# Kernel optimization log

Measured on AMD Instinct MI355X. Metric: run time of the kernel, lower is better.

## Reference

```python
import jax, jax.numpy as jnp
import numpy as np

B, N, K, PC, NC = 4, 4096, 20, 6, 13


def setup_inputs() -> dict:
    key = jax.random.key(0)
    ks = jax.random.split(key, 32)
    dims = [(12, 64), (64, 64), (128, 64), (64, 64), (128, 64), (192, 1024), (1216, 512), (512, 256)]
    inp = {"x": jax.random.normal(ks[0], (B, N, PC), jnp.float32)}
    for j, (ci, co) in enumerate(dims, 1):
        inp[f"w{j}"] = jax.random.normal(ks[j], (co, ci), jnp.float32) * (1.0 / np.sqrt(ci))
        # BatchNorm (eval mode) folded to per-channel affine: y = h*s + b
        inp[f"s{j}"] = jnp.ones((co,), jnp.float32) + 0.01 * jax.random.normal(ks[10 + j], (co,), jnp.float32)
        inp[f"b{j}"] = 0.01 * jax.random.normal(ks[20 + j], (co,), jnp.float32)
    inp["w9"] = jax.random.normal(ks[30], (NC, 256), jnp.float32) * (1.0 / np.sqrt(256))
    inp["b9"] = 0.01 * jax.random.normal(ks[31], (NC,), jnp.float32)
    return inp


def _lrelu(h):
    return jnp.where(h >= 0, h, 0.2 * h)


def _knn_idx(y, k):
    # y: (B, C, N); pairwise_distance = -||xi - xj||^2, topk -> nearest neighbors
    xx = jnp.sum(y * y, axis=1)                       # (B, N)
    inner = jnp.einsum('bcn,bcm->bnm', y, y)          # (B, N, N)
    pd = 2.0 * inner - xx[:, :, None] - xx[:, None, :]
    return jax.lax.top_k(pd, k)[1]                    # (B, N, k) int32


def _graph_feature(y, k):
    # y: (B, C, N) -> edge features (B, 2C, N, k): concat(neighbor - x, x)
    idx = _knn_idx(y, k)
    yt = jnp.transpose(y, (0, 2, 1))                  # (B, N, C)
    nb = jax.vmap(lambda f, i: f[i])(yt, idx)         # (B, N, k, C)
    c = yt[:, :, None, :]
    feat = jnp.concatenate([nb - c, jnp.broadcast_to(c, nb.shape)], axis=-1)
    return jnp.transpose(feat, (0, 3, 1, 2))          # (B, 2C, N, k)


def _conv2(f, w, s, b):
    # 1x1 Conv2d (no bias) + folded BN + LeakyReLU(0.2)
    h = jnp.einsum('oc,bcnk->bonk', w, f)
    return _lrelu(h * s[None, :, None, None] + b[None, :, None, None])


def _conv1(f, w, s, b):
    h = jnp.einsum('oc,bcn->bon', w, f)
    return _lrelu(h * s[None, :, None] + b[None, :, None])


def _forward(x, w1, s1, b1, w2, s2, b2, w3, s3, b3, w4, s4, b4, w5, s5, b5,
             w6, s6, b6, w7, s7, b7, w8, s8, b8, w9, b9):
    y = jnp.transpose(x, (0, 2, 1))                   # (B, C, N)
    f = _graph_feature(y, K)
    h = _conv2(f, w1, s1, b1)
    h = _conv2(h, w2, s2, b2)
    x1 = h.max(axis=-1)                               # (B, 64, N)
    f = _graph_feature(x1, K)
    h = _conv2(f, w3, s3, b3)
    h = _conv2(h, w4, s4, b4)
    x2 = h.max(axis=-1)
    f = _graph_feature(x2, K)
    h = _conv2(f, w5, s5, b5)
    x3 = h.max(axis=-1)
    cat = jnp.concatenate([x1, x2, x3], axis=1)       # (B, 192, N)
    g = _conv1(cat, w6, s6, b6).max(axis=-1, keepdims=True)  # (B, 1024, 1)
    g = jnp.broadcast_to(g, (g.shape[0], g.shape[1], x1.shape[-1]))
    h = jnp.concatenate([g, x1, x2, x3], axis=1)      # (B, 1216, N)
    h = _conv1(h, w7, s7, b7)
    h = _conv1(h, w8, s8, b8)
    # dropout is identity in eval mode
    out = jnp.einsum('oc,bcn->bon', w9, h) + b9[None, :, None]
    return out                                        # (B, NC, N)


def reference(x, w1, s1, b1, w2, s2, b2, w3, s3, b3, w4, s4, b4, w5, s5, b5,
              w6, s6, b6, w7, s7, b7, w8, s8, b8, w9, b9):
    return _forward(x, w1, s1, b1, w2, s2, b2, w3, s3, b3, w4, s4, b4, w5, s5, b5,
                    w6, s6, b6, w7, s7, b7, w8, s8, b8, w9, b9)
```

## Files before the change

kernel.cpp:

```cpp
#include <hip/hip_runtime.h>
#include <hip/hip_bf16.h>
#include <cstdint>
#include <cstddef>

#define NB 4
#define NPTS 4096
#define KK 20

typedef unsigned int u32;
typedef unsigned long long u64;

__device__ __forceinline__ float lrelu(float v) { return v >= 0.f ? v : 0.2f * v; }

__device__ __forceinline__ u32 fmap(float f) {
  u32 u = __float_as_uint(f);
  return (int)u < 0 ? ~u : (u | 0x80000000u);
}

__device__ __forceinline__ u64 wmax64(u64 v) {
#pragma unroll
  for (int o = 32; o >= 1; o >>= 1) {
    u64 t = __shfl_xor(v, o, 64);
    v = t > v ? t : v;
  }
  return v;
}

template <int C>
__global__ void k_sq(const float* __restrict__ f, float* __restrict__ xx) {
  int p = blockIdx.x * 256 + threadIdx.x;
  const float* fp = f + (size_t)p * C;
  float s = 0.f;
  if constexpr ((C & 3) == 0) {
#pragma unroll
    for (int c = 0; c < C; c += 4) {
      float4 v = *reinterpret_cast<const float4*>(fp + c);
      s += v.x * v.x + v.y * v.y + v.z * v.z + v.w * v.w;
    }
  } else {
#pragma unroll
    for (int c = 0; c < C; c++) s += fp[c] * fp[c];
  }
  xx[p] = s;
}

__global__ __launch_bounds__(512) void k_knn6(const float* __restrict__ f,
                                              const float* __restrict__ xx,
                                              int* __restrict__ idxo,
                                              int* __restrict__ flg) {
  __shared__ float chunkl[6 * 65];
  const int tid = threadIdx.x, wv = tid >> 6, lane = tid & 63;
  const int row = blockIdx.x * 8 + wv;
  const int b = row >> 12;
  const float xi = xx[row];

  float y[6];
#pragma unroll
  for (int c = 0; c < 6; c++) y[c] = f[(size_t)row * 6 + c];

  u64 t0 = 0, t1 = 0, t2 = 0, t3 = 0;

  for (int jc = 0; jc < NPTS / 64; jc++) {
    __syncthreads();
    for (int t = tid; t < 64 * 6; t += 512) {
      int j = t / 6, c = t - j * 6;
      chunkl[c * 65 + j] = f[(size_t)(b * NPTS + jc * 64 + j) * 6 + c];
    }
    __syncthreads();
    const float xj = xx[b * NPTS + jc * 64 + lane];
    float acc = 0.f;
#pragma unroll
    for (int c = 0; c < 6; c++) acc = fmaf(chunkl[c * 65 + lane], y[c], acc);
    const float s = fmaf(2.f, acc, -xi) - xj;
    const u64 key = ((u64)fmap(s) << 32) | (u64)(~(u32)(jc * 64 + lane));
    if (key > t3) {
      u64 a0 = t0, a1 = t1, a2 = t2;
      bool g0 = key > a0, g1 = key > a1, g2 = key > a2;
      t0 = g0 ? key : a0;
      t1 = g0 ? a0 : (g1 ? key : a1);
      t2 = g1 ? a1 : (g2 ? key : a2);
      t3 = g2 ? a2 : key;
    }
  }

  u64 h = t0, n1 = t1, n2 = t2, n3 = t3;
  int pops = 0, myj = 0;
  for (int m = 0; m < KK; m++) {
    u64 wm = wmax64(h);
    int j = (int)(~(u32)wm) & (NPTS - 1);
    if (lane == m) myj = j;
    if (h == wm) { h = n1; n1 = n2; n2 = n3; n3 = 0; pops++; }
  }
  u64 bad = __ballot(pops >= 4);
  if (lane < KK) idxo[(size_t)row * KK + lane] = myj;
  if (lane == 0) flg[row] = (bad != 0ull) ? 1 : 0;
}

__global__ __launch_bounds__(256, 2) void k_knn64(const float* __restrict__ f,
                                                  const float* __restrict__ xx,
                                                  int* __restrict__ idxo,
                                                  int* __restrict__ flg) {
  __shared__ float ch[2][64 * 68];
  __shared__ float ypl[16 * 68];
  const int tid = threadIdx.x, wv = tid >> 6, lane = tid & 63;
  const int rowbase = blockIdx.x * 16;
  const int b = rowbase >> 12;
  const float* fb = f + (size_t)b * NPTS * 64;
  const int r0 = rowbase + wv * 4;

  {
    int row = tid >> 4, q = tid & 15;
    float4 v = *reinterpret_cast<const float4*>(f + (size_t)(rowbase + row) * 64 + 4 * q);
    *reinterpret_cast<float4*>(&ypl[row * 68 + 4 * q]) = v;
  }
  float xi[4];
#pragma unroll
  for (int r = 0; r < 4; r++) xi[r] = xx[r0 + r];

  u64 t0[4], t1[4], t2[4], t3[4];
#pragma unroll
  for (int r = 0; r < 4; r++) { t0[r] = 0; t1[r] = 0; t2[r] = 0; t3[r] = 0; }

#pragma unroll 1
  for (int jp = 0; jp < NPTS / 128; jp++) {
#pragma unroll 1
    for (int k = 0; k < 8; k++) {
      int flat = k * 256 + tid;
      int row = flat >> 4, q = flat & 15;
      float4 v = *reinterpret_cast<const float4*>(
          fb + (size_t)(jp * 128 + row) * 64 + 4 * q);
      *reinterpret_cast<float4*>(&ch[row >> 6][(row & 63) * 68 + 4 * q]) = v;
    }
    __syncthreads();

    float acc[4][2];
#pragma unroll
    for (int r = 0; r < 4; r++) { acc[r][0] = 0.f; acc[r][1] = 0.f; }
#pragma unroll 2
    for (int q = 0; q < 16; q++) {
      const float4 c0 = *reinterpret_cast<const float4*>(&ch[0][lane * 68 + 4 * q]);
      const float4 c1 = *reinterpret_cast<const float4*>(&ch[1][lane * 68 + 4 * q]);
#pragma unroll
      for (int r = 0; r < 4; r++) {
        const float4 yq = *reinterpret_cast<const float4*>(&ypl[(wv * 4 + r) * 68 + 4 * q]);
        acc[r][0] = fmaf(c0.x, yq.x, acc[r][0]);
        acc[r][0] = fmaf(c0.y, yq.y, acc[r][0]);
        acc[r][0] = fmaf(c0.z, yq.z, acc[r][0]);
        acc[r][0] = fmaf(c0.w, yq.w, acc[r][0]);
        acc[r][1] = fmaf(c1.x, yq.x, acc[r][1]);
        acc[r][1] = fmaf(c1.y, yq.y, acc[r][1]);
        acc[r][1] = fmaf(c1.z, yq.z, acc[r][1]);
        acc[r][1] = fmaf(c1.w, yq.w, acc[r][1]);
      }
    }
    const float xj0 = xx[b * NPTS + jp * 128 + lane];
    const float xj1 = xx[b * NPTS + jp * 128 + 64 + lane];
    const u32 j0 = ~(u32)(jp * 128 + lane);
    const u32 j1 = ~(u32)(jp * 128 + 64 + lane);
#pragma unroll
    for (int r = 0; r < 4; r++) {
      {
        const float s = fmaf(2.f, acc[r][0], -xi[r]) - xj0;
        const u64 key = ((u64)fmap(s) << 32) | (u64)j0;
        if (key > t3[r]) {
          u64 a0 = t0[r], a1 = t1[r], a2 = t2[r];
          bool g0 = key > a0, g1 = key > a1, g2 = key > a2;
          t0[r] = g0 ? key : a0;
          t1[r] = g0 ? a0 : (g1 ? key : a1);
          t2[r] = g1 ? a1 : (g2 ? key : a2);
          t3[r] = g2 ? a2 : key;
        }
      }
      {
        const float s = fmaf(2.f, acc[r][1], -xi[r]) - xj1;
        const u64 key = ((u64)fmap(s) << 32) | (u64)j1;
        if (key > t3[r]) {
          u64 a0 = t0[r], a1 = t1[r], a2 = t2[r];
          bool g0 = key > a0, g1 = key > a1, g2 = key > a2;
          t0[r] = g0 ? key : a0;
          t1[r] = g0 ? a0 : (g1 ? key : a1);
          t2[r] = g1 ? a1 : (g2 ? key : a2);
          t3[r] = g2 ? a2 : key;
        }
      }
    }
    __syncthreads();
  }

#pragma unroll
  for (int r = 0; r < 4; r++) {
    u64 h = t0[r], n1 = t1[r], n2 = t2[r], n3 = t3[r];
    int pops = 0, myj = 0;
    for (int m = 0; m < KK; m++) {
      u64 wm = wmax64(h);
      int j = (int)(~(u32)wm) & (NPTS - 1);
      if (lane == m) myj = j;
      if (h == wm) { h = n1; n1 = n2; n2 = n3; n3 = 0; pops++; }
    }
    u64 bad = __ballot(pops >= 4);
    if (lane < KK) idxo[(size_t)(r0 + r) * KK + lane] = myj;
    if (lane == 0) flg[r0 + r] = (bad != 0ull) ? 1 : 0;
  }
}

template <int C>
__global__ __launch_bounds__(64) void k_knn_fix(const float* __restrict__ f,
                                                const float* __restrict__ xx,
                                                int* __restrict__ idxo,
                                                const int* __restrict__ flg) {
  __shared__ u64 kl[NPTS];
  const int lane = threadIdx.x;
  for (int row = blockIdx.x; row < NB * NPTS; row += gridDim.x) {
    if (!flg[row]) continue;
    const int b = row >> 12;
    float yreg[C];
#pragma unroll
    for (int c = 0; c < C; c++) yreg[c] = f[(size_t)row * C + c];
    const float xi = xx[row];
    for (int jj = 0; jj < 64; jj++) {
      int j = jj * 64 + lane;
      const float* fp = f + (size_t)(b * NPTS + j) * C;
      float d = 0.f;
#pragma unroll
      for (int c = 0; c < C; c++) d = fmaf(yreg[c], fp[c], d);
      float s = fmaf(2.f, d, -xi) - xx[b * NPTS + j];
      kl[j] = ((u64)fmap(s) << 32) | (u64)(u32)(~(u32)j);
    }
    __syncthreads();
    int myj = 0;
    for (int m = 0; m < KK; m++) {
      u64 lm = 0;
      for (int jj = 0; jj < 64; jj++) {
        u64 v = kl[jj * 64 + lane];
        lm = v > lm ? v : lm;
      }
      u64 wm = wmax64(lm);
      int j = (int)(~(u32)wm) & (NPTS - 1);
      if (lane == m) myj = j;
      if (lane == (j & 63)) kl[j] = 0;
      __syncthreads();
    }
    if (lane < KK) idxo[row * KK + lane] = myj;
    __syncthreads();
  }
}

__global__ __launch_bounds__(256) void k_ec1(
    const float* __restrict__ x, const int* __restrict__ idx,
    const float* __restrict__ w1, const float* __restrict__ s1, const float* __restrict__ b1,
    const float* __restrict__ w2, const float* __restrict__ s2, const float* __restrict__ b2,
    float* __restrict__ out) {
  __shared__ float h1l[4][64];
  const int wv = threadIdx.x >> 6, lane = threadIdx.x & 63;
  float w1r[12];
#pragma unroll
  for (int c = 0; c < 12; c += 4) {
    float4 v = *reinterpret_cast<const float4*>(w1 + lane * 12 + c);
    w1r[c] = v.x; w1r[c + 1] = v.y; w1r[c + 2] = v.z; w1r[c + 3] = v.w;
  }
  float w2r[64];
#pragma unroll
  for (int c = 0; c < 64; c += 4) {
    float4 v = *reinterpret_cast<const float4*>(w2 + lane * 64 + c);
    w2r[c] = v.x; w2r[c + 1] = v.y; w2r[c + 2] = v.z; w2r[c + 3] = v.w;
  }
  const float sc1 = s1[lane], bc1 = b1[lane], sc2 = s2[lane], bc2 = b2[lane];
  const int wid = blockIdx.x * 4 + wv;
  for (int p = wid; p < NB * NPTS; p += 2048) {
    const float* cp = x + (size_t)p * 6;
    float c0 = cp[0], c1 = cp[1], c2 = cp[2], c3 = cp[3], c4 = cp[4], c5 = cp[5];
    const int bb = p >> 12;
    float m = -3.402823466e38f;
    for (int k = 0; k < KK; k++) {
      int nb = idx[p * KK + k];
      const float* nf = x + (size_t)((bb << 12) + nb) * 6;
      float e0 = nf[0] - c0, e1 = nf[1] - c1, e2 = nf[2] - c2;
      float e3 = nf[3] - c3, e4 = nf[4] - c4, e5 = nf[5] - c5;
      float h = w1r[0] * e0 + w1r[1] * e1 + w1r[2] * e2 + w1r[3] * e3 + w1r[4] * e4 +
                w1r[5] * e5 + w1r[6] * c0 + w1r[7] * c1 + w1r[8] * c2 + w1r[9] * c3 +
                w1r[10] * c4 + w1r[11] * c5;
      h = lrelu(fmaf(h, sc1, bc1));
      h1l[wv][lane] = h;
      __syncthreads();
      float a0 = 0.f, a1 = 0.f;
#pragma unroll
      for (int c = 0; c < 64; c += 8) {
        float4 hv = *reinterpret_cast<const float4*>(&h1l[wv][c]);
        float4 hw = *reinterpret_cast<const float4*>(&h1l[wv][c + 4]);
        a0 = fmaf(w2r[c], hv.x, a0); a0 = fmaf(w2r[c + 1], hv.y, a0);
        a0 = fmaf(w2r[c + 2], hv.z, a0); a0 = fmaf(w2r[c + 3], hv.w, a0);
        a1 = fmaf(w2r[c + 4], hw.x, a1); a1 = fmaf(w2r[c + 5], hw.y, a1);
        a1 = fmaf(w2r[c + 6], hw.z, a1); a1 = fmaf(w2r[c + 7], hw.w, a1);
      }
      m = fmaxf(m, lrelu(fmaf(a0 + a1, sc2, bc2)));
      __syncthreads();
    }
    out[(size_t)p * 64 + lane] = m;
  }
}

template <bool HAS2>
__global__ __launch_bounds__(256, 1) void k_ec2(
    const float* __restrict__ xin, const int* __restrict__ idx,
    const float* __restrict__ w3, const float* __restrict__ s3, const float* __restrict__ b3,
    const float* __restrict__ w4, const float* __restrict__ s4, const float* __restrict__ b4,
    float* __restrict__ out) {
  __shared__ float ctl[4][64];
  __shared__ float nbl[4][64];
  __shared__ float h1l[4][64];
  const int wv = threadIdx.x >> 6, lane = threadIdx.x & 63;
  float wa[64], wb[64];
#pragma unroll
  for (int c = 0; c < 64; c += 4) {
    float4 va = *reinterpret_cast<const float4*>(w3 + (size_t)lane * 128 + c);
    float4 vb = *reinterpret_cast<const float4*>(w3 + (size_t)lane * 128 + 64 + c);
    wa[c] = va.x; wa[c + 1] = va.y; wa[c + 2] = va.z; wa[c + 3] = va.w;
    wb[c] = vb.x - va.x; wb[c + 1] = vb.y - va.y; wb[c + 2] = vb.z - va.z; wb[c + 3] = vb.w - va.w;
  }
  float w4r[64];
  if constexpr (HAS2) {
#pragma unroll
    for (int c = 0; c < 64; c += 4) {
      float4 v = *reinterpret_cast<const float4*>(w4 + (size_t)lane * 64 + c);
      w4r[c] = v.x; w4r[c + 1] = v.y; w4r[c + 2] = v.z; w4r[c + 3] = v.w;
    }
  }
  const float sc3 = s3[lane], bc3 = b3[lane];
  float sc4 = 0.f, bc4 = 0.f;
  if constexpr (HAS2) { sc4 = s4[lane]; bc4 = b4[lane]; }
  const int wid = blockIdx.x * 4 + wv;
  for (int p = wid; p < NB * NPTS; p += 2048) {
    const int bb = p >> 12;
    ctl[wv][lane] = xin[(size_t)p * 64 + lane];
    __syncthreads();
    float d0 = 0.f, d1 = 0.f;
#pragma unroll
    for (int c = 0; c < 64; c += 8) {
      float4 cv = *reinterpret_cast<const float4*>(&ctl[wv][c]);
      float4 cw = *reinterpret_cast<const float4*>(&ctl[wv][c + 4]);
      d0 = fmaf(wb[c], cv.x, d0); d0 = fmaf(wb[c + 1], cv.y, d0);
      d0 = fmaf(wb[c + 2], cv.z, d0); d0 = fmaf(wb[c + 3], cv.w, d0);
      d1 = fmaf(wb[c + 4], cw.x, d1); d1 = fmaf(wb[c + 5], cw.y, d1);
      d1 = fmaf(wb[c + 6], cw.z, d1); d1 = fmaf(wb[c + 7], cw.w, d1);
    }
    const float cd = d0 + d1;
    float m = -3.402823466e38f;
    for (int k = 0; k < KK; k++) {
      int nb = idx[p * KK + k];
      nbl[wv][lane] = xin[(size_t)((bb << 12) + nb) * 64 + lane];
      __syncthreads();
      float a0 = cd, a1 = 0.f;
#pragma unroll
      for (int c = 0; c < 64; c += 8) {
        float4 nv = *reinterpret_cast<const float4*>(&nbl[wv][c]);
        float4 nw = *reinterpret_cast<const float4*>(&nbl[wv][c + 4]);
        a0 = fmaf(wa[c], nv.x, a0); a0 = fmaf(wa[c + 1], nv.y, a0);
        a0 = fmaf(wa[c + 2], nv.z, a0); a0 = fmaf(wa[c + 3], nv.w, a0);
        a1 = fmaf(wa[c + 4], nw.x, a1); a1 = fmaf(wa[c + 5], nw.y, a1);
        a1 = fmaf(wa[c + 6], nw.z, a1); a1 = fmaf(wa[c + 7], nw.w, a1);
      }
      float h = lrelu(fmaf(a0 + a1, sc3, bc3));
      if constexpr (HAS2) {
        h1l[wv][lane] = h;
        __syncthreads();
        float q0 = 0.f, q1 = 0.f;
#pragma unroll
        for (int c = 0; c < 64; c += 8) {
          float4 hv = *reinterpret_cast<const float4*>(&h1l[wv][c]);
          float4 hw = *reinterpret_cast<const float4*>(&h1l[wv][c + 4]);
          q0 = fmaf(w4r[c], hv.x, q0); q0 = fmaf(w4r[c + 1], hv.y, q0);
          q0 = fmaf(w4r[c + 2], hv.z, q0); q0 = fmaf(w4r[c + 3], hv.w, q0);
          q1 = fmaf(w4r[c + 4], hw.x, q1); q1 = fmaf(w4r[c + 5], hw.y, q1);
          q1 = fmaf(w4r[c + 6], hw.z, q1); q1 = fmaf(w4r[c + 7], hw.w, q1);
        }
        m = fmaxf(m, lrelu(fmaf(q0 + q1, sc4, bc4)));
        __syncthreads();
      } else {
        m = fmaxf(m, h);
        __syncthreads();
      }
    }
    out[(size_t)p * 64 + lane] = m;
    __syncthreads();
  }
}

__global__ __launch_bounds__(256, 1) void k_conv6(
    const float* __restrict__ x1, const float* __restrict__ x2, const float* __restrict__ x3,
    const float* __restrict__ w6, const float* __restrict__ s6, const float* __restrict__ b6,
    float* __restrict__ gpart) {
  __shared__ float fl[192];
  const int tid = threadIdx.x;
  const int cg = blockIdx.x & 3;
  const int ch = (blockIdx.x >> 2) & 31;
  const int b = blockIdx.x >> 7;
  const int co = cg * 256 + tid;
  float wr[192];
#pragma unroll
  for (int c = 0; c < 192; c += 4) {
    float4 v = *reinterpret_cast<const float4*>(w6 + (size_t)co * 192 + c);
    wr[c] = v.x; wr[c + 1] = v.y; wr[c + 2] = v.z; wr[c + 3] = v.w;
  }
  const float sc = s6[co], bc = b6[co];
  float m = -3.402823466e38f;
  for (int pp = 0; pp < 128; pp++) {
    const int p = b * NPTS + ch * 128 + pp;
    if (tid < 192) {
      fl[tid] = tid < 64 ? x1[(size_t)p * 64 + tid]
              : tid < 128 ? x2[(size_t)p * 64 + tid - 64]
                          : x3[(size_t)p * 64 + tid - 128];
    }
    __syncthreads();
    float a0 = 0.f, a1 = 0.f, a2 = 0.f, a3 = 0.f;
#pragma unroll
    for (int c = 0; c < 192; c += 16) {
      float4 f0 = *reinterpret_cast<const float4*>(&fl[c]);
      float4 f1 = *reinterpret_cast<const float4*>(&fl[c + 4]);
      float4 f2 = *reinterpret_cast<const float4*>(&fl[c + 8]);
      float4 f3 = *reinterpret_cast<const float4*>(&fl[c + 12]);
      a0 = fmaf(wr[c], f0.x, a0); a0 = fmaf(wr[c + 1], f0.y, a0);
      a0 = fmaf(wr[c + 2], f0.z, a0); a0 = fmaf(wr[c + 3], f0.w, a0);
      a1 = fmaf(wr[c + 4], f1.x, a1); a1 = fmaf(wr[c + 5], f1.y, a1);
      a1 = fmaf(wr[c + 6], f1.z, a1); a1 = fmaf(wr[c + 7], f1.w, a1);
      a2 = fmaf(wr[c + 8], f2.x, a2); a2 = fmaf(wr[c + 9], f2.y, a2);
      a2 = fmaf(wr[c + 10], f2.z, a2); a2 = fmaf(wr[c + 11], f2.w, a2);
      a3 = fmaf(wr[c + 12], f3.x, a3); a3 = fmaf(wr[c + 13], f3.y, a3);
      a3 = fmaf(wr[c + 14], f3.z, a3); a3 = fmaf(wr[c + 15], f3.w, a3);
    }
    m = fmaxf(m, lrelu(fmaf((a0 + a1) + (a2 + a3), sc, bc)));
    __syncthreads();
  }
  gpart[(size_t)(b * 32 + ch) * 1024 + co] = m;
}

__global__ void k_gred(const float* __restrict__ gpart, float* __restrict__ g) {
  int t = blockIdx.x * 256 + threadIdx.x;
  int b = t >> 10, co = t & 1023;
  float m = -3.402823466e38f;
  for (int ch = 0; ch < 32; ch++) m = fmaxf(m, gpart[(size_t)(b * 32 + ch) * 1024 + co]);
  g[t] = m;
}

__global__ void k_gc(const float* __restrict__ w7, const float* __restrict__ g,
                     float* __restrict__ gcv) {
  int t = blockIdx.x * 256 + threadIdx.x;
  int b = t >> 9, co = t & 511;
  const float* gr = g + b * 1024;
  const float* wr = w7 + (size_t)co * 1216;
  float a0 = 0.f, a1 = 0.f, a2 = 0.f, a3 = 0.f;
  for (int ci = 0; ci < 1024; ci += 4) {
    float4 wv = *reinterpret_cast<const float4*>(wr + ci);
    float4 gv = *reinterpret_cast<const float4*>(gr + ci);
    a0 = fmaf(wv.x, gv.x, a0); a1 = fmaf(wv.y, gv.y, a1);
    a2 = fmaf(wv.z, gv.z, a2); a3 = fmaf(wv.w, gv.w, a3);
  }
  gcv[t] = (a0 + a1) + (a2 + a3);
}

__global__ __launch_bounds__(256, 1) void k_conv7(
    const float* __restrict__ x1, const float* __restrict__ x2, const float* __restrict__ x3,
    const float* __restrict__ gcv, const float* __restrict__ w7,
    const float* __restrict__ s7, const float* __restrict__ b7,
    float* __restrict__ h7, int bbase) {
  __shared__ float fl[192];
  const int tid = threadIdx.x;
  const int wv = tid >> 6, lane = tid & 63;
  const int cohalf = blockIdx.x & 1;
  const int ch = (blockIdx.x >> 1) & 63;
  const int bloc = blockIdx.x >> 7;
  const int b = bbase + bloc;
  const int co = (cohalf * 4 + wv) * 64 + lane;
  float wr[192];
#pragma unroll
  for (int c = 0; c < 192; c += 4) {
    float4 v = *reinterpret_cast<const float4*>(w7 + (size_t)co * 1216 + 1024 + c);
    wr[c] = v.x; wr[c + 1] = v.y; wr[c + 2] = v.z; wr[c + 3] = v.w;
  }
  const float sc = s7[co], bc = b7[co], g0 = gcv[b * 512 + co];
  for (int pp = 0; pp < 64; pp++) {
    const int p = b * NPTS + ch * 64 + pp;
    if (tid < 192) {
      fl[tid] = tid < 64 ? x1[(size_t)p * 64 + tid]
              : tid < 128 ? x2[(size_t)p * 64 + tid - 64]
                          : x3[(size_t)p * 64 + tid - 128];
    }
    __syncthreads();
    float a0 = g0, a1 = 0.f, a2 = 0.f, a3 = 0.f;
#pragma unroll
    for (int c = 0; c < 192; c += 16) {
      float4 f0 = *reinterpret_cast<const float4*>(&fl[c]);
      float4 f1 = *reinterpret_cast<const float4*>(&fl[c + 4]);
      float4 f2 = *reinterpret_cast<const float4*>(&fl[c + 8]);
      float4 f3 = *reinterpret_cast<const float4*>(&fl[c + 12]);
      a0 = fmaf(wr[c], f0.x, a0); a0 = fmaf(wr[c + 1], f0.y, a0);
      a0 = fmaf(wr[c + 2], f0.z, a0); a0 = fmaf(wr[c + 3], f0.w, a0);
      a1 = fmaf(wr[c + 4], f1.x, a1); a1 = fmaf(wr[c + 5], f1.y, a1);
      a1 = fmaf(wr[c + 6], f1.z, a1); a1 = fmaf(wr[c + 7], f1.w, a1);
      a2 = fmaf(wr[c + 8], f2.x, a2); a2 = fmaf(wr[c + 9], f2.y, a2);
      a2 = fmaf(wr[c + 10], f2.z, a2); a2 = fmaf(wr[c + 11], f2.w, a2);
      a3 = fmaf(wr[c + 12], f3.x, a3); a3 = fmaf(wr[c + 13], f3.y, a3);
      a3 = fmaf(wr[c + 14], f3.z, a3); a3 = fmaf(wr[c + 15], f3.w, a3);
    }
    h7[(size_t)(bloc * NPTS + ch * 64 + pp) * 512 + co] =
        lrelu(fmaf((a0 + a1) + (a2 + a3), sc, bc));
    __syncthreads();
  }
}

__global__ __launch_bounds__(256) void k_conv8(
    const float* __restrict__ h7, const float* __restrict__ w8,
    const float* __restrict__ s8, const float* __restrict__ b8,
    float* __restrict__ h8, int bbase) {
  __shared__ float Wl[64 * 68];
  __shared__ float Xl[64 * 68];
  const int tid = threadIdx.x;
  const int cot = blockIdx.x & 3;
  const int nt = blockIdx.x >> 2;
  const int co0 = (tid & 15) * 4;
  const int n0 = (tid >> 4) * 4;
  const int sr = tid >> 2;
  const int sci = (tid & 3) * 16;
  float acc[4][4];
#pragma unroll
  for (int i = 0; i < 4; i++)
#pragma unroll
    for (int j = 0; j < 4; j++) acc[i][j] = 0.f;

  for (int cib = 0; cib < 512; cib += 64) {
    __syncthreads();
    {
      const float* ws_ = w8 + (size_t)(cot * 64 + sr) * 512 + cib + sci;
#pragma unroll
      for (int s = 0; s < 16; s += 4) {
        float4 v = *reinterpret_cast<const float4*>(ws_ + s);
        Wl[(sci + s) * 68 + sr] = v.x;
        Wl[(sci + s + 1) * 68 + sr] = v.y;
        Wl[(sci + s + 2) * 68 + sr] = v.z;
        Wl[(sci + s + 3) * 68 + sr] = v.w;
      }
      const float* xs = h7 + (size_t)(nt * 64 + sr) * 512 + cib + sci;
#pragma unroll
      for (int s = 0; s < 16; s += 4) {
        float4 v = *reinterpret_cast<const float4*>(xs + s);
        Xl[(sci + s) * 68 + sr] = v.x;
        Xl[(sci + s + 1) * 68 + sr] = v.y;
        Xl[(sci + s + 2) * 68 + sr] = v.z;
        Xl[(sci + s + 3) * 68 + sr] = v.w;
      }
    }
    __syncthreads();
#pragma unroll 8
    for (int ci = 0; ci < 64; ci++) {
      float4 wv = *reinterpret_cast<const float4*>(&Wl[ci * 68 + co0]);
      float4 xv = *reinterpret_cast<const float4*>(&Xl[ci * 68 + n0]);
      acc[0][0] = fmaf(wv.x, xv.x, acc[0][0]);
      acc[0][1] = fmaf(wv.x, xv.y, acc[0][1]);
      acc[0][2] = fmaf(wv.x, xv.z, acc[0][2]);
      acc[0][3] = fmaf(wv.x, xv.w, acc[0][3]);
      acc[1][0] = fmaf(wv.y, xv.x, acc[1][0]);
      acc[1][1] = fmaf(wv.y, xv.y, acc[1][1]);
      acc[1][2] = fmaf(wv.y, xv.z, acc[1][2]);
      acc[1][3] = fmaf(wv.y, xv.w, acc[1][3]);
      acc[2][0] = fmaf(wv.z, xv.x, acc[2][0]);
      acc[2][1] = fmaf(wv.z, xv.y, acc[2][1]);
      acc[2][2] = fmaf(wv.z, xv.z, acc[2][2]);
      acc[2][3] = fmaf(wv.z, xv.w, acc[2][3]);
      acc[3][0] = fmaf(wv.w, xv.x, acc[3][0]);
      acc[3][1] = fmaf(wv.w, xv.y, acc[3][1]);
      acc[3][2] = fmaf(wv.w, xv.z, acc[3][2]);
      acc[3][3] = fmaf(wv.w, xv.w, acc[3][3]);
    }
  }
  float scv[4], bcv[4];
#pragma unroll
  for (int i = 0; i < 4; i++) {
    scv[i] = s8[cot * 64 + co0 + i];
    bcv[i] = b8[cot * 64 + co0 + i];
  }
#pragma unroll
  for (int j = 0; j < 4; j++) {
    float4 o;
    o.x = lrelu(fmaf(acc[0][j], scv[0], bcv[0]));
    o.y = lrelu(fmaf(acc[1][j], scv[1], bcv[1]));
    o.z = lrelu(fmaf(acc[2][j], scv[2], bcv[2]));
    o.w = lrelu(fmaf(acc[3][j], scv[3], bcv[3]));
    *reinterpret_cast<float4*>(
        &h8[(size_t)(bbase * NPTS + nt * 64 + n0 + j) * 256 + cot * 64 + co0]) = o;
  }
}

__global__ __launch_bounds__(256) void k_conv9(const float* __restrict__ h8,
                                               const float* __restrict__ w9,
                                               const float* __restrict__ b9,
                                               float* __restrict__ outp) {
  __shared__ float Wl[16 * 256];
  __shared__ float Xl[64 * 68];
  const int tid = threadIdx.x;
  for (int q = tid; q < 16 * 256; q += 256) Wl[q] = q < 13 * 256 ? w9[q] : 0.f;
  const int p = tid & 63, cg = tid >> 6;
  const int sr = tid >> 2, sci = (tid & 3) * 16;
  float acc[4] = {0.f, 0.f, 0.f, 0.f};
  for (int cib = 0; cib < 256; cib += 64) {
    __syncthreads();
    {
      const float* xs = h8 + (size_t)(blockIdx.x * 64 + sr) * 256 + cib + sci;
#pragma unroll
      for (int s = 0; s < 16; s += 4) {
        float4 v = *reinterpret_cast<const float4*>(xs + s);
        Xl[(sci + s) * 68 + sr] = v.x;
        Xl[(sci + s + 1) * 68 + sr] = v.y;
        Xl[(sci + s + 2) * 68 + sr] = v.z;
        Xl[(sci + s + 3) * 68 + sr] = v.w;
      }
    }
    __syncthreads();
#pragma unroll 8
    for (int ci = 0; ci < 64; ci++) {
      float xv = Xl[ci * 68 + p];
#pragma unroll
      for (int q = 0; q < 4; q++)
        acc[q] = fmaf(Wl[(cg * 4 + q) * 256 + cib + ci], xv, acc[q]);
    }
  }
  const int pg = blockIdx.x * 64 + p;
  const int bb = pg >> 12, n = pg & (NPTS - 1);
#pragma unroll
  for (int q = 0; q < 4; q++) {
    int co = cg * 4 + q;
    if (co < 13) outp[(size_t)(bb * 13 + co) * NPTS + n] = acc[q] + b9[co];
  }
}

extern "C" void kernel_launch(void* const* d_in, const int* in_sizes, int n_in,
                              void* d_out, int out_size, void* d_ws, size_t ws_size,
                              hipStream_t stream) {
  const float* x = (const float*)d_in[0];
  const float* w1 = (const float*)d_in[1];
  const float* s1 = (const float*)d_in[2];
  const float* b1 = (const float*)d_in[3];
  const float* w2 = (const float*)d_in[4];
  const float* s2 = (const float*)d_in[5];
  const float* b2 = (const float*)d_in[6];
  const float* w3 = (const float*)d_in[7];
  const float* s3 = (const float*)d_in[8];
  const float* b3 = (const float*)d_in[9];
  const float* w4 = (const float*)d_in[10];
  const float* s4 = (const float*)d_in[11];
  const float* b4 = (const float*)d_in[12];
  const float* w5 = (const float*)d_in[13];
  const float* s5 = (const float*)d_in[14];
  const float* b5 = (const float*)d_in[15];
  const float* w6 = (const float*)d_in[16];
  const float* s6 = (const float*)d_in[17];
  const float* b6 = (const float*)d_in[18];
  const float* w7 = (const float*)d_in[19];
  const float* s7 = (const float*)d_in[20];
  const float* b7 = (const float*)d_in[21];
  const float* w8 = (const float*)d_in[22];
  const float* s8 = (const float*)d_in[23];
  const float* b8 = (const float*)d_in[24];
  const float* w9 = (const float*)d_in[25];
  const float* b9 = (const float*)d_in[26];

  float* ws = (float*)d_ws;
  float* xxp = ws + 0;
  int* idxp = (int*)(ws + 16384);
  int* flg = (int*)(ws + 344064);
  float* x1 = ws + 360448;
  float* x2 = ws + 1409024;
  float* x3 = ws + 2457600;
  float* gpart = ws + 3506176;
  float* g = ws + 3637248;
  float* gcv = ws + 3641344;
  float* h7 = ws + 3643392;
  float* h8 = ws + 7837696;

  k_sq<6><<<64, 256, 0, stream>>>(x, xxp);
  k_knn6<<<2048, 512, 0, stream>>>(x, xxp, idxp, flg);
  k_knn_fix<6><<<512, 64, 0, stream>>>(x, xxp, idxp, flg);
  k_ec1<<<512, 256, 0, stream>>>(x, idxp, w1, s1, b1, w2, s2, b2, x1);
  k_sq<64><<<64, 256, 0, stream>>>(x1, xxp);
  k_knn64<<<1024, 256, 0, stream>>>(x1, xxp, idxp, flg);
  k_knn_fix<64><<<512, 64, 0, stream>>>(x1, xxp, idxp, flg);
  k_ec2<true><<<512, 256, 0, stream>>>(x1, idxp, w3, s3, b3, w4, s4, b4, x2);
  k_sq<64><<<64, 256, 0, stream>>>(x2, xxp);
  k_knn64<<<1024, 256, 0, stream>>>(x2, xxp, idxp, flg);
  k_knn_fix<64><<<512, 64, 0, stream>>>(x2, xxp, idxp, flg);
  k_ec2<false><<<512, 256, 0, stream>>>(x2, idxp, w5, s5, b5, nullptr, nullptr, nullptr, x3);
  k_conv6<<<512, 256, 0, stream>>>(x1, x2, x3, w6, s6, b6, gpart);
  k_gred<<<16, 256, 0, stream>>>(gpart, g);
  k_gc<<<8, 256, 0, stream>>>(w7, g, gcv);
  for (int bbase = 0; bbase < NB; bbase += 2) {
    k_conv7<<<256, 256, 0, stream>>>(x1, x2, x3, gcv, w7, s7, b7, h7, bbase);
    k_conv8<<<512, 256, 0, stream>>>(h7, w8, s8, b8, h8, bbase);
  }
  k_conv9<<<256, 256, 0, stream>>>(h8, w9, b9, (float*)d_out);
}
```

Baseline: 2.221 ms.

## Tile conv6/conv7 as shared-memory register-blocked GEMMs and drop wave-local block barriers

```diff
diff --git a/kernel.cpp b/kernel.cpp
--- a/kernel.cpp
+++ b/kernel.cpp
@@ -281,7 +281,6 @@
                 w1r[10] * c4 + w1r[11] * c5;
       h = lrelu(fmaf(h, sc1, bc1));
       h1l[wv][lane] = h;
-      __syncthreads();
       float a0 = 0.f, a1 = 0.f;
 #pragma unroll
       for (int c = 0; c < 64; c += 8) {
@@ -293,7 +292,6 @@
         a1 = fmaf(w2r[c + 6], hw.z, a1); a1 = fmaf(w2r[c + 7], hw.w, a1);
       }
       m = fmaxf(m, lrelu(fmaf(a0 + a1, sc2, bc2)));
-      __syncthreads();
     }
     out[(size_t)p * 64 + lane] = m;
   }
@@ -332,7 +330,6 @@
   for (int p = wid; p < NB * NPTS; p += 2048) {
     const int bb = p >> 12;
     ctl[wv][lane] = xin[(size_t)p * 64 + lane];
-    __syncthreads();
     float d0 = 0.f, d1 = 0.f;
 #pragma unroll
     for (int c = 0; c < 64; c += 8) {
@@ -348,7 +345,6 @@
     for (int k = 0; k < KK; k++) {
       int nb = idx[p * KK + k];
       nbl[wv][lane] = xin[(size_t)((bb << 12) + nb) * 64 + lane];
-      __syncthreads();
       float a0 = cd, a1 = 0.f;
 #pragma unroll
       for (int c = 0; c < 64; c += 8) {
@@ -362,7 +358,6 @@
       float h = lrelu(fmaf(a0 + a1, sc3, bc3));
       if constexpr (HAS2) {
         h1l[wv][lane] = h;
-        __syncthreads();
         float q0 = 0.f, q1 = 0.f;
 #pragma unroll
         for (int c = 0; c < 64; c += 8) {
@@ -374,63 +369,107 @@
           q1 = fmaf(w4r[c + 6], hw.z, q1); q1 = fmaf(w4r[c + 7], hw.w, q1);
         }
         m = fmaxf(m, lrelu(fmaf(q0 + q1, sc4, bc4)));
-        __syncthreads();
       } else {
         m = fmaxf(m, h);
-        __syncthreads();
       }
     }
     out[(size_t)p * 64 + lane] = m;
-    __syncthreads();
-  }
-}
-
-__global__ __launch_bounds__(256, 1) void k_conv6(
+  }
+}
+
+__global__ __launch_bounds__(256) void k_conv6(
     const float* __restrict__ x1, const float* __restrict__ x2, const float* __restrict__ x3,
     const float* __restrict__ w6, const float* __restrict__ s6, const float* __restrict__ b6,
     float* __restrict__ gpart) {
-  __shared__ float fl[192];
+  __shared__ float Wl[64 * 68];
+  __shared__ float Xl[64 * 68];
+  __shared__ float mxl[16][64];
   const int tid = threadIdx.x;
-  const int cg = blockIdx.x & 3;
-  const int ch = (blockIdx.x >> 2) & 31;
-  const int b = blockIdx.x >> 7;
-  const int co = cg * 256 + tid;
-  float wr[192];
-#pragma unroll
-  for (int c = 0; c < 192; c += 4) {
-    float4 v = *reinterpret_cast<const float4*>(w6 + (size_t)co * 192 + c);
-    wr[c] = v.x; wr[c + 1] = v.y; wr[c + 2] = v.z; wr[c + 3] = v.w;
-  }
-  const float sc = s6[co], bc = b6[co];
-  float m = -3.402823466e38f;
-  for (int pp = 0; pp < 128; pp++) {
-    const int p = b * NPTS + ch * 128 + pp;
-    if (tid < 192) {
-      fl[tid] = tid < 64 ? x1[(size_t)p * 64 + tid]
-              : tid < 128 ? x2[(size_t)p * 64 + tid - 64]
-                          : x3[(size_t)p * 64 + tid - 128];
-    }
-    __syncthreads();
-    float a0 = 0.f, a1 = 0.f, a2 = 0.f, a3 = 0.f;
-#pragma unroll
-    for (int c = 0; c < 192; c += 16) {
-      float4 f0 = *reinterpret_cast<const float4*>(&fl[c]);
-      float4 f1 = *reinterpret_cast<const float4*>(&fl[c + 4]);
-      float4 f2 = *reinterpret_cast<const float4*>(&fl[c + 8]);
-      float4 f3 = *reinterpret_cast<const float4*>(&fl[c + 12]);
-      a0 = fmaf(wr[c], f0.x, a0); a0 = fmaf(wr[c + 1], f0.y, a0);
-      a0 = fmaf(wr[c + 2], f0.z, a0); a0 = fmaf(wr[c + 3], f0.w, a0);
-      a1 = fmaf(wr[c + 4], f1.x, a1); a1 = fmaf(wr[c + 5], f1.y, a1);
-      a1 = fmaf(wr[c + 6], f1.z, a1); a1 = fmaf(wr[c + 7], f1.w, a1);
-      a2 = fmaf(wr[c + 8], f2.x, a2); a2 = fmaf(wr[c + 9], f2.y, a2);
-      a2 = fmaf(wr[c + 10], f2.z, a2); a2 = fmaf(wr[c + 11], f2.w, a2);
-      a3 = fmaf(wr[c + 12], f3.x, a3); a3 = fmaf(wr[c + 13], f3.y, a3);
-      a3 = fmaf(wr[c + 14], f3.z, a3); a3 = fmaf(wr[c + 15], f3.w, a3);
-    }
-    m = fmaxf(m, lrelu(fmaf((a0 + a1) + (a2 + a3), sc, bc)));
-    __syncthreads();
-  }
-  gpart[(size_t)(b * 32 + ch) * 1024 + co] = m;
+  const int cot = blockIdx.x & 15;
+  const int ptb = blockIdx.x >> 4;
+  const int co0 = (tid & 15) * 4;
+  const int n0 = (tid >> 4) * 4;
+  const int sr = tid >> 2;
+  const int sci = (tid & 3) * 16;
+  float scv[4], bcv[4];
+#pragma unroll
+  for (int i = 0; i < 4; i++) {
+    scv[i] = s6[cot * 64 + co0 + i];
+    bcv[i] = b6[cot * 64 + co0 + i];
+  }
+  float mx[4];
+#pragma unroll
+  for (int i = 0; i < 4; i++) mx[i] = -3.402823466e38f;
+
+  for (int half = 0; half < 2; half++) {
+    float acc[4][4];
+#pragma unroll
+    for (int i = 0; i < 4; i++)
+#pragma unroll
+      for (int j = 0; j < 4; j++) acc[i][j] = 0.f;
+    for (int cib = 0; cib < 3; cib++) {
+      const float* xsel = cib == 0 ? x1 : cib == 1 ? x2 : x3;
+      __syncthreads();
+      {
+        const float* ws_ = w6 + (size_t)(cot * 64 + sr) * 192 + cib * 64 + sci;
+#pragma unroll
+        for (int s = 0; s < 16; s += 4) {
+          float4 v = *reinterpret_cast<const float4*>(ws_ + s);
+          Wl[(sci + s) * 68 + sr] = v.x;
+          Wl[(sci + s + 1) * 68 + sr] = v.y;
+          Wl[(sci + s + 2) * 68 + sr] = v.z;
+          Wl[(sci + s + 3) * 68 + sr] = v.w;
+        }
+        const float* xs = xsel + (size_t)(ptb * 128 + half * 64 + sr) * 64 + sci;
+#pragma unroll
+        for (int s = 0; s < 16; s += 4) {
+          float4 v = *reinterpret_cast<const float4*>(xs + s);
+          Xl[(sci + s) * 68 + sr] = v.x;
+          Xl[(sci + s + 1) * 68 + sr] = v.y;
+          Xl[(sci + s + 2) * 68 + sr] = v.z;
+          Xl[(sci + s + 3) * 68 + sr] = v.w;
+        }
+      }
+      __syncthreads();
+#pragma unroll 8
+      for (int ci = 0; ci < 64; ci++) {
+        float4 wv = *reinterpret_cast<const float4*>(&Wl[ci * 68 + co0]);
+        float4 xv = *reinterpret_cast<const float4*>(&Xl[ci * 68 + n0]);
+        acc[0][0] = fmaf(wv.x, xv.x, acc[0][0]);
+        acc[0][1] = fmaf(wv.x, xv.y, acc[0][1]);
+        acc[0][2] = fmaf(wv.x, xv.z, acc[0][2]);
+        acc[0][3] = fmaf(wv.x, xv.w, acc[0][3]);
+        acc[1][0] = fmaf(wv.y, xv.x, acc[1][0]);
+        acc[1][1] = fmaf(wv.y, xv.y, acc[1][1]);
+        acc[1][2] = fmaf(wv.y, xv.z, acc[1][2]);
+        acc[1][3] = fmaf(wv.y, xv.w, acc[1][3]);
+        acc[2][0] = fmaf(wv.z, xv.x, acc[2][0]);
+        acc[2][1] = fmaf(wv.z, xv.y, acc[2][1]);
+        acc[2][2] = fmaf(wv.z, xv.z, acc[2][2]);
+        acc[2][3] = fmaf(wv.z, xv.w, acc[2][3]);
+        acc[3][0] = fmaf(wv.w, xv.x, acc[3][0]);
+        acc[3][1] = fmaf(wv.w, xv.y, acc[3][1]);
+        acc[3][2] = fmaf(wv.w, xv.z, acc[3][2]);
+        acc[3][3] = fmaf(wv.w, xv.w, acc[3][3]);
+      }
+    }
+#pragma unroll
+    for (int i = 0; i < 4; i++)
+#pragma unroll
+      for (int j = 0; j < 4; j++)
+        mx[i] = fmaxf(mx[i], lrelu(fmaf(acc[i][j], scv[i], bcv[i])));
+  }
+  __syncthreads();
+#pragma unroll
+  for (int i = 0; i < 4; i++) mxl[tid >> 4][co0 + i] = mx[i];
+  __syncthreads();
+  if (tid < 64) {
+    float m = -3.402823466e38f;
+#pragma unroll
+    for (int g = 0; g < 16; g++) m = fmaxf(m, mxl[g][tid]);
+    const int b = ptb >> 5, ch = ptb & 31;
+    gpart[(size_t)(b * 32 + ch) * 1024 + cot * 64 + tid] = m;
+  }
 }
 
 __global__ void k_gred(const float* __restrict__ gpart, float* __restrict__ g) {
@@ -457,53 +496,89 @@
   gcv[t] = (a0 + a1) + (a2 + a3);
 }
 
-__global__ __launch_bounds__(256, 1) void k_conv7(
+__global__ __launch_bounds__(256) void k_conv7(
     const float* __restrict__ x1, const float* __restrict__ x2, const float* __restrict__ x3,
     const float* __restrict__ gcv, const float* __restrict__ w7,
     const float* __restrict__ s7, const float* __restrict__ b7,
     float* __restrict__ h7, int bbase) {
-  __shared__ float fl[192];
+  __shared__ float Wl[64 * 68];
+  __shared__ float Xl[64 * 68];
   const int tid = threadIdx.x;
-  const int wv = tid >> 6, lane = tid & 63;
-  const int cohalf = blockIdx.x & 1;
-  const int ch = (blockIdx.x >> 1) & 63;
-  const int bloc = blockIdx.x >> 7;
-  const int b = bbase + bloc;
-  const int co = (cohalf * 4 + wv) * 64 + lane;
-  float wr[192];
-#pragma unroll
-  for (int c = 0; c < 192; c += 4) {
-    float4 v = *reinterpret_cast<const float4*>(w7 + (size_t)co * 1216 + 1024 + c);
-    wr[c] = v.x; wr[c + 1] = v.y; wr[c + 2] = v.z; wr[c + 3] = v.w;
-  }
-  const float sc = s7[co], bc = b7[co], g0 = gcv[b * 512 + co];
-  for (int pp = 0; pp < 64; pp++) {
-    const int p = b * NPTS + ch * 64 + pp;
-    if (tid < 192) {
-      fl[tid] = tid < 64 ? x1[(size_t)p * 64 + tid]
-              : tid < 128 ? x2[(size_t)p * 64 + tid - 64]
-                          : x3[(size_t)p * 64 + tid - 128];
-    }
-    __syncthreads();
-    float a0 = g0, a1 = 0.f, a2 = 0.f, a3 = 0.f;
-#pragma unroll
-    for (int c = 0; c < 192; c += 16) {
-      float4 f0 = *reinterpret_cast<const float4*>(&fl[c]);
-      float4 f1 = *reinterpret_cast<const float4*>(&fl[c + 4]);
-      float4 f2 = *reinterpret_cast<const float4*>(&fl[c + 8]);
-      float4 f3 = *reinterpret_cast<const float4*>(&fl[c + 12]);
-      a0 = fmaf(wr[c], f0.x, a0); a0 = fmaf(wr[c + 1], f0.y, a0);
-      a0 = fmaf(wr[c + 2], f0.z, a0); a0 = fmaf(wr[c + 3], f0.w, a0);
-      a1 = fmaf(wr[c + 4], f1.x, a1); a1 = fmaf(wr[c + 5], f1.y, a1);
-      a1 = fmaf(wr[c + 6], f1.z, a1); a1 = fmaf(wr[c + 7], f1.w, a1);
-      a2 = fmaf(wr[c + 8], f2.x, a2); a2 = fmaf(wr[c + 9], f2.y, a2);
-      a2 = fmaf(wr[c + 10], f2.z, a2); a2 = fmaf(wr[c + 11], f2.w, a2);
-      a3 = fmaf(wr[c + 12], f3.x, a3); a3 = fmaf(wr[c + 13], f3.y, a3);
-      a3 = fmaf(wr[c + 14], f3.z, a3); a3 = fmaf(wr[c + 15], f3.w, a3);
-    }
-    h7[(size_t)(bloc * NPTS + ch * 64 + pp) * 512 + co] =
-        lrelu(fmaf((a0 + a1) + (a2 + a3), sc, bc));
-    __syncthreads();
+  const int cot = blockIdx.x & 7;
+  const int nt = blockIdx.x >> 3;
+  const int co0 = (tid & 15) * 4;
+  const int n0 = (tid >> 4) * 4;
+  const int sr = tid >> 2;
+  const int sci = (tid & 3) * 16;
+  float acc[4][4];
+#pragma unroll
+  for (int i = 0; i < 4; i++)
+#pragma unroll
+    for (int j = 0; j < 4; j++) acc[i][j] = 0.f;
+
+  for (int cib = 0; cib < 3; cib++) {
+    const float* xsel = cib == 0 ? x1 : cib == 1 ? x2 : x3;
+    __syncthreads();
+    {
+      const float* ws_ = w7 + (size_t)(cot * 64 + sr) * 1216 + 1024 + cib * 64 + sci;
+#pragma unroll
+      for (int s = 0; s < 16; s += 4) {
+        float4 v = *reinterpret_cast<const float4*>(ws_ + s);
+        Wl[(sci + s) * 68 + sr] = v.x;
+        Wl[(sci + s + 1) * 68 + sr] = v.y;
+        Wl[(sci + s + 2) * 68 + sr] = v.z;
+        Wl[(sci + s + 3) * 68 + sr] = v.w;
+      }
+      const float* xs = xsel + (size_t)(bbase * NPTS + nt * 64 + sr) * 64 + sci;
+#pragma unroll
+      for (int s = 0; s < 16; s += 4) {
+        float4 v = *reinterpret_cast<const float4*>(xs + s);
+        Xl[(sci + s) * 68 + sr] = v.x;
+        Xl[(sci + s + 1) * 68 + sr] = v.y;
+        Xl[(sci + s + 2) * 68 + sr] = v.z;
+        Xl[(sci + s + 3) * 68 + sr] = v.w;
+      }
+    }
+    __syncthreads();
+#pragma unroll 8
+    for (int ci = 0; ci < 64; ci++) {
+      float4 wv = *reinterpret_cast<const float4*>(&Wl[ci * 68 + co0]);
+      float4 xv = *reinterpret_cast<const float4*>(&Xl[ci * 68 + n0]);
+      acc[0][0] = fmaf(wv.x, xv.x, acc[0][0]);
+      acc[0][1] = fmaf(wv.x, xv.y, acc[0][1]);
+      acc[0][2] = fmaf(wv.x, xv.z, acc[0][2]);
+      acc[0][3] = fmaf(wv.x, xv.w, acc[0][3]);
+      acc[1][0] = fmaf(wv.y, xv.x, acc[1][0]);
+      acc[1][1] = fmaf(wv.y, xv.y, acc[1][1]);
+      acc[1][2] = fmaf(wv.y, xv.z, acc[1][2]);
+      acc[1][3] = fmaf(wv.y, xv.w, acc[1][3]);
+      acc[2][0] = fmaf(wv.z, xv.x, acc[2][0]);
+      acc[2][1] = fmaf(wv.z, xv.y, acc[2][1]);
+      acc[2][2] = fmaf(wv.z, xv.z, acc[2][2]);
+      acc[2][3] = fmaf(wv.z, xv.w, acc[2][3]);
+      acc[3][0] = fmaf(wv.w, xv.x, acc[3][0]);
+      acc[3][1] = fmaf(wv.w, xv.y, acc[3][1]);
+      acc[3][2] = fmaf(wv.w, xv.z, acc[3][2]);
+      acc[3][3] = fmaf(wv.w, xv.w, acc[3][3]);
+    }
+  }
+  const int b = bbase + (nt >> 6);
+  float scv[4], bcv[4], g0v[4];
+#pragma unroll
+  for (int i = 0; i < 4; i++) {
+    scv[i] = s7[cot * 64 + co0 + i];
+    bcv[i] = b7[cot * 64 + co0 + i];
+    g0v[i] = gcv[b * 512 + cot * 64 + co0 + i];
+  }
+#pragma unroll
+  for (int j = 0; j < 4; j++) {
+    float4 o;
+    o.x = lrelu(fmaf(acc[0][j] + g0v[0], scv[0], bcv[0]));
+    o.y = lrelu(fmaf(acc[1][j] + g0v[1], scv[1], bcv[1]));
+    o.z = lrelu(fmaf(acc[2][j] + g0v[2], scv[2], bcv[2]));
+    o.w = lrelu(fmaf(acc[3][j] + g0v[3], scv[3], bcv[3]));
+    *reinterpret_cast<float4*>(
+        &h7[(size_t)(nt * 64 + n0 + j) * 512 + cot * 64 + co0]) = o;
   }
 }
 
@@ -687,11 +762,11 @@
   k_knn64<<<1024, 256, 0, stream>>>(x2, xxp, idxp, flg);
   k_knn_fix<64><<<512, 64, 0, stream>>>(x2, xxp, idxp, flg);
   k_ec2<false><<<512, 256, 0, stream>>>(x2, idxp, w5, s5, b5, nullptr, nullptr, nullptr, x3);
-  k_conv6<<<512, 256, 0, stream>>>(x1, x2, x3, w6, s6, b6, gpart);
+  k_conv6<<<2048, 256, 0, stream>>>(x1, x2, x3, w6, s6, b6, gpart);
   k_gred<<<16, 256, 0, stream>>>(gpart, g);
   k_gc<<<8, 256, 0, stream>>>(w7, g, gcv);
   for (int bbase = 0; bbase < NB; bbase += 2) {
-    k_conv7<<<256, 256, 0, stream>>>(x1, x2, x3, gcv, w7, s7, b7, h7, bbase);
+    k_conv7<<<1024, 256, 0, stream>>>(x1, x2, x3, gcv, w7, s7, b7, h7, bbase);
     k_conv8<<<512, 256, 0, stream>>>(h7, w8, s8, b8, h8, bbase);
   }
   k_conv9<<<256, 256, 0, stream>>>(h8, w9, b9, (float*)d_out);
```

New measurement: 1.907 ms. 1.16x faster.
